# Kernel optimization log

Hardware: AMD Instinct MI355X
Metric: run time of the kernel (lower is better)

## Reference

```python
import jax, jax.numpy as jnp
import numpy as np

B, K, V, NB = 256, 62, 14522, 28

def setup_inputs() -> dict:
    key = jax.random.key(0)
    ks = jax.random.split(key, 10)
    thetas = jax.random.normal(ks[0], (B, K * 3), dtype=jnp.float32) * 0.2
    bone_lengths_core = jax.random.normal(ks[1], (B, NB), dtype=jnp.float32)
    center_bone_length = jax.random.uniform(ks[2], (B, 1), dtype=jnp.float32) + 0.5
    trans = jax.random.normal(ks[3], (B, 3), dtype=jnp.float32)
    scale = jax.random.uniform(ks[4], (B,), dtype=jnp.float32) + 0.5
    v_template = jax.random.normal(ks[5], (V, 3), dtype=jnp.float32) * 0.05
    t_pose_joints = jax.random.normal(ks[6], (K, 3), dtype=jnp.float32) * 0.1
    weights = jax.nn.softmax(jax.random.normal(ks[7], (V, K), dtype=jnp.float32) * 2.0, axis=1)
    # kinematic tree: parent[i] < i (binary-ish tree), parent[0] unused
    parents = jnp.maximum((jnp.arange(K) - 1) // 2, 0).astype(jnp.int64)
    bone_length_mapper = jax.random.randint(ks[8], (K,), -1, NB).astype(jnp.int64)
    return {"thetas": thetas, "bone_lengths_core": bone_lengths_core,
            "center_bone_length": center_bone_length, "trans": trans, "scale": scale,
            "v_template": v_template, "t_pose_joints": t_pose_joints, "weights": weights,
            "parents": parents, "bone_length_mapper": bone_length_mapper}

def euler2mat(r):
    # r: [N,3] ZYX euler angles -> [N,3,3]
    z, y, x = r[:, 0], r[:, 1], r[:, 2]
    cx, sx = jnp.cos(x), jnp.sin(x)
    cy, sy = jnp.cos(y), jnp.sin(y)
    cz, sz = jnp.cos(z), jnp.sin(z)
    one = jnp.ones_like(x)
    zero = jnp.zeros_like(x)
    Rx = jnp.stack([one, zero, zero, zero, cx, -sx, zero, sx, cx], -1).reshape(-1, 3, 3)
    Ry = jnp.stack([cy, zero, sy, zero, one, zero, -sy, zero, cy], -1).reshape(-1, 3, 3)
    Rz = jnp.stack([cz, -sz, zero, sz, cz, zero, zero, zero, one], -1).reshape(-1, 3, 3)
    return jnp.einsum('nij,njk,nkl->nil', Rz, Ry, Rx)

def _forward(thetas, bone_lengths_core, center_bone_length, trans, scale,
             v_template, t_pose_joints, weights, parents, bone_length_mapper):
    b = thetas.shape[0]
    k = t_pose_joints.shape[0]
    blc = jax.nn.sigmoid(bone_lengths_core / 5.0) * 2.0          # [B,28]
    R = euler2mat(thetas.reshape(-1, 3)).reshape(b, k, 3, 3)      # [B,K,3,3]
    Jt = t_pose_joints                                            # [K,3]
    # per-joint bone-length scale factor [B,K]
    gathered = blc[:, jnp.clip(bone_length_mapper, 0)]            # [B,K]
    factor = jnp.where(bone_length_mapper[None, :] < 0, 1.0, gathered)
    factor = factor.at[:, 1].set(center_bone_length[:, 0])
    factor = factor.at[:, 0].set(1.0)
    # local translations: root uses J0, others scaled offsets to parent
    off = (Jt - Jt[parents])[None] * factor[:, :, None]           # [B,K,3]
    off = off.at[:, 0].set(Jt[0][None])
    # local affines A [B,K,4,4]
    A = jnp.zeros((b, k, 4, 4), dtype=thetas.dtype)
    A = A.at[:, :, :3, :3].set(R)
    A = A.at[:, :, :3, 3].set(off)
    A = A.at[:, :, 3, 3].set(1.0)
    # compose along the kinematic tree
    G0 = jnp.zeros_like(A).at[:, 0].set(A[:, 0])
    def step(G_all, i):
        Gp = jnp.take(G_all, parents[i], axis=1)                  # [B,4,4]
        Gi = Gp @ jnp.take(A, i, axis=1)
        return jax.lax.dynamic_update_index_in_dim(G_all, Gi, i, axis=1), None
    G_all, _ = jax.lax.scan(step, G0, jnp.arange(1, k))
    J_final = G_all[:, :, :3, 3]                                  # [B,K,3]
    # subtract inverse-bind contribution: G' = G - pack(G @ [J;0])
    RJ = jnp.einsum('bkij,kj->bki', G_all[:, :, :3, :3], Jt)
    G = G_all.at[:, :, :3, 3].add(-RJ)
    # LBS skinning: T [B,V,4,4]
    T = jnp.einsum('bkij,vk->bvij', G, weights)
    rest_h = jnp.concatenate([v_template, jnp.ones((v_template.shape[0], 1), v_template.dtype)], axis=1)
    v = jnp.einsum('bvij,vj->bvi', T, rest_h)[:, :, :3]
    V_final = v * scale[:, None, None] + trans[:, None, :]
    J_out = J_final * scale[:, None, None] + trans[:, None, :]
    return V_final, J_out

def reference(thetas, bone_lengths_core, center_bone_length, trans, scale,
              v_template, t_pose_joints, weights, parents, bone_length_mapper):
    return _forward(thetas, bone_lengths_core, center_bone_length, trans, scale,
                    v_template, t_pose_joints, weights, parents, bone_length_mapper)
```

## Files before the change

kernel.cpp:

```cpp
#include <hip/hip_runtime.h>

#define NJ     62
#define NV     14522
#define NCORE  28
#define KPAD   256
#define OUTF   (NV * 3)
#define MT     908
#define NSTR   192

typedef __attribute__((ext_vector_type(8))) short short8v;
typedef __attribute__((ext_vector_type(4))) short short4v;
typedef __attribute__((ext_vector_type(4))) float floatx4;
typedef __attribute__((ext_vector_type(2))) float floatx2;

#define AS1(p) ((const __attribute__((address_space(1))) void*)(p))
#define AS3(p) ((__attribute__((address_space(3))) void*)(p))

#define SCHED0() __builtin_amdgcn_sched_barrier(0)
#define WAITVM0() do { SCHED0(); asm volatile("s_waitcnt vmcnt(0)" ::: "memory"); SCHED0(); } while (0)

static __device__ inline short f2bf(float x) {
    unsigned u = __float_as_uint(x);
    unsigned r = (u + 0x7fffu + ((u >> 16) & 1u)) >> 16;
    return (short)r;
}

static __device__ inline short8v pack8(float a0, float a1, float a2, float a3,
                                       float a4, float a5, float a6, float a7) {
    union { unsigned u[4]; short8v v; } p;
    asm("v_cvt_pk_bf16_f32 %0, %1, %2" : "=v"(p.u[0]) : "v"(a0), "v"(a1));
    asm("v_cvt_pk_bf16_f32 %0, %1, %2" : "=v"(p.u[1]) : "v"(a2), "v"(a3));
    asm("v_cvt_pk_bf16_f32 %0, %1, %2" : "=v"(p.u[2]) : "v"(a4), "v"(a5));
    asm("v_cvt_pk_bf16_f32 %0, %1, %2" : "=v"(p.u[3]) : "v"(a6), "v"(a7));
    return p.v;
}

static __device__ inline unsigned swz(unsigned off) {
    return off ^ (((off >> 9) & 7u) << 4);
}

__global__ __launch_bounds__(256) void fk_kernel(
    const float* __restrict__ thetas, const float* __restrict__ blc,
    const float* __restrict__ cbl, const float* __restrict__ trans,
    const float* __restrict__ scale, const float* __restrict__ tpose,
    const int* __restrict__ parents, const int* __restrict__ mapper,
    short* __restrict__ Bt, float* __restrict__ Jout)
{
    __shared__ float Asm[4][NJ][12];
    __shared__ float Gsm[4][NJ][12];

    const int w = threadIdx.x >> 6;
    const int b = blockIdx.x * 4 + w;
    const int k = threadIdx.x & 63;
    int p = 0;

    if (k < NJ) {
        p = parents[k];
        const float tz = thetas[(b * NJ + k) * 3 + 0];
        const float ty = thetas[(b * NJ + k) * 3 + 1];
        const float tx = thetas[(b * NJ + k) * 3 + 2];
        const float cx = cosf(tx), sx = sinf(tx);
        const float cy = cosf(ty), sy = sinf(ty);
        const float cz = cosf(tz), sz = sinf(tz);
        const float r00 = cz * cy;
        const float r01 = cz * sy * sx - sz * cx;
        const float r02 = sz * sx + cz * sy * cx;
        const float r10 = sz * cy;
        const float r11 = cz * cx + sz * sy * sx;
        const float r12 = sz * sy * cx - cz * sx;
        const float r20 = -sy;
        const float r21 = cy * sx;
        const float r22 = cy * cx;

        float f;
        const int m = mapper[k];
        if (k == 0)        f = 1.0f;
        else if (k == 1)   f = cbl[b];
        else if (m < 0)    f = 1.0f;
        else               f = 2.0f / (1.0f + expf(-blc[b * NCORE + m] * 0.2f));

        float ox, oy, oz;
        if (k == 0) {
            ox = tpose[0]; oy = tpose[1]; oz = tpose[2];
        } else {
            ox = (tpose[k * 3 + 0] - tpose[p * 3 + 0]) * f;
            oy = (tpose[k * 3 + 1] - tpose[p * 3 + 1]) * f;
            oz = (tpose[k * 3 + 2] - tpose[p * 3 + 2]) * f;
        }
        Asm[w][k][0] = r00; Asm[w][k][1] = r01; Asm[w][k][2]  = r02; Asm[w][k][3]  = ox;
        Asm[w][k][4] = r10; Asm[w][k][5] = r11; Asm[w][k][6]  = r12; Asm[w][k][7]  = oy;
        Asm[w][k][8] = r20; Asm[w][k][9] = r21; Asm[w][k][10] = r22; Asm[w][k][11] = oz;
    }
    __syncthreads();

    if (k == 0) {
        #pragma unroll
        for (int j = 0; j < 12; ++j) Gsm[w][0][j] = Asm[w][0][j];
    }
    __syncthreads();

    const int depth = (k < NJ) ? (31 - __clz((unsigned)(k + 1))) : 99;
    for (int d = 1; d <= 5; ++d) {
        if (depth == d) {
            float gp[12], a[12], g[12];
            #pragma unroll
            for (int j = 0; j < 12; ++j) { gp[j] = Gsm[w][p][j]; a[j] = Asm[w][k][j]; }
            #pragma unroll
            for (int i = 0; i < 3; ++i) {
                #pragma unroll
                for (int j = 0; j < 4; ++j) {
                    float s = (j == 3) ? gp[i * 4 + 3] : 0.0f;
                    s = fmaf(gp[i * 4 + 0], a[0 * 4 + j], s);
                    s = fmaf(gp[i * 4 + 1], a[1 * 4 + j], s);
                    s = fmaf(gp[i * 4 + 2], a[2 * 4 + j], s);
                    g[i * 4 + j] = s;
                }
            }
            #pragma unroll
            for (int j = 0; j < 12; ++j) Gsm[w][k][j] = g[j];
        }
        __syncthreads();
    }

    if (k < NJ) {
        float g[12];
        #pragma unroll
        for (int j = 0; j < 12; ++j) g[j] = Gsm[w][k][j];
        const float jx = tpose[k * 3 + 0];
        const float jy = tpose[k * 3 + 1];
        const float jz = tpose[k * 3 + 2];
        const float s  = scale[b];
        Jout[(b * NJ + k) * 3 + 0] = fmaf(g[3],  s, trans[b * 3 + 0]);
        Jout[(b * NJ + k) * 3 + 1] = fmaf(g[7],  s, trans[b * 3 + 1]);
        Jout[(b * NJ + k) * 3 + 2] = fmaf(g[11], s, trans[b * 3 + 2]);
        float np[3];
        np[0] = g[3]  - (g[0] * jx + g[1] * jy + g[2]  * jz);
        np[1] = g[7]  - (g[4] * jx + g[5] * jy + g[6]  * jz);
        np[2] = g[11] - (g[8] * jx + g[9] * jy + g[10] * jz);

        const int lkj = k >> 4;
        const int rr  = k & 15;
        const int qb  = 32 * (rr >> 1) + 8 * lkj + 4 * (rr & 1);
        #pragma unroll
        for (int i = 0; i < 3; ++i) {
            short4v o;
            o[0] = f2bf(g[i * 4 + 0]);
            o[1] = f2bf(g[i * 4 + 1]);
            o[2] = f2bf(g[i * 4 + 2]);
            o[3] = f2bf(np[i]);
            *(short4v*)&Bt[(size_t)(b * 3 + i) * KPAD + qb] = o;
        }
        if (k == 0) {
            short4v z = {0, 0, 0, 0};
            #pragma unroll
            for (int i = 0; i < 3; ++i) {
                *(short4v*)&Bt[(size_t)(b * 3 + i) * KPAD + 248] = z;
                *(short4v*)&Bt[(size_t)(b * 3 + i) * KPAD + 252] = z;
            }
        }
    }
}

__global__ __launch_bounds__(256, 3) void gemm_skin(
    const float* __restrict__ W,
    const float* __restrict__ vt,
    const short* __restrict__ Bt,
    const float* __restrict__ scale,
    const float* __restrict__ trans,
    float* __restrict__ out)
{
    __shared__ __align__(16) char ldsB[48 * 512];
    __shared__ __align__(16) float epi_all[4 * 1600];

    const int tid  = threadIdx.x;
    const int wave = tid >> 6;
    const int lane = tid & 63;
    const int lrow = lane & 15;
    const int lk   = lane >> 4;
    const int yy    = blockIdx.x / 48;
    const int inner = blockIdx.x - yy * 48;
    const int s     = inner * 4 + wave;
    const int start  = s * 4 + (s < 140 ? s : 140);
    const int ntiles = 4 + (s < 140 ? 1 : 0);
    const int b0 = yy * 16;
    float* epi0 = epi_all + wave * 1600;
    float* epi1 = epi0 + 800;

    {
        const char* Bsrc = (const char*)(Bt + (size_t)yy * 48 * KPAD);
        #pragma unroll
        for (int cc = 0; cc < 6; ++cc) {
            const unsigned Lb = (unsigned)(wave * 6144 + cc * 1024);
            __builtin_amdgcn_global_load_lds(AS1(Bsrc + swz(Lb + lane * 16)),
                                             AS3(ldsB + Lb), 16, 0, 0);
        }
    }

    float sv[3], tv[3]; int eoff[3];
    #pragma unroll
    for (int nt = 0; nt < 3; ++nt) {
        const int n_loc = nt * 16 + lrow;
        const int bl = n_loc / 3, ii = n_loc - bl * 3;
        eoff[nt] = bl * 50 + ii;
        sv[nt] = scale[b0 + bl];
        tv[nt] = trans[(b0 + bl) * 3 + ii];
    }
    unsigned bofs[3], bxor[3];
    #pragma unroll
    for (int nt = 0; nt < 3; ++nt) {
        const unsigned brow = nt * 16 + lrow;
        bofs[nt] = brow * 512;
        bxor[nt] = (brow & 7u) << 4;
    }

    auto do_store = [&](int tt, const float* ebuf) {
        const int m48 = (start + tt) * 48;
        const bool edge = (m48 + 48 > OUTF);
        #pragma unroll
        for (int it = 0; it < 6; ++it) {
            const int idx = it * 64 + lane;
            const int r = idx / 24, j = idx - r * 24;
            const floatx2 val = *(const floatx2*)&ebuf[r * 50 + 2 * j];
            const int pp = m48 + 2 * j;
            if (!edge || pp + 1 < OUTF)
                *(floatx2*)&out[(size_t)(b0 + r) * OUTF + pp] = val;
        }
    };

    floatx4 wc[4]; float hcx, hcy, hcz;
    {
        int vrow = start * 16 + lrow;
        if (vrow > NV - 1) vrow = NV - 1;
        const float* Wb = W + (size_t)vrow * NJ + lk * 16;
        wc[0] = *(const floatx4*)(Wb + 0);
        wc[1] = *(const floatx4*)(Wb + 4);
        wc[2] = *(const floatx4*)(Wb + 8);
        wc[3] = *(const floatx4*)(Wb + 12);
        hcx = vt[vrow * 3 + 0]; hcy = vt[vrow * 3 + 1]; hcz = vt[vrow * 3 + 2];
    }

    WAITVM0();
    __syncthreads();

    for (int t = 0; t < ntiles; ++t) {
        float* ecur = (t & 1) ? epi1 : epi0;

        if (t > 0) do_store(t - 1, (t & 1) ? epi0 : epi1);

        floatx4 wn[4]; float hnx = 0.f, hny = 0.f, hnz = 0.f;
        if (t + 1 < ntiles) {
            int vr = (start + t + 1) * 16 + lrow;
            if (vr > NV - 1) vr = NV - 1;
            const float* Wb = W + (size_t)vr * NJ + lk * 16;
            wn[0] = *(const floatx4*)(Wb + 0);
            wn[1] = *(const floatx4*)(Wb + 4);
            wn[2] = *(const floatx4*)(Wb + 8);
            wn[3] = *(const floatx4*)(Wb + 12);
            hnx = vt[vr * 3 + 0]; hny = vt[vr * 3 + 1]; hnz = vt[vr * 3 + 2];
        } else {
            wn[0] = wn[1] = wn[2] = wn[3] = (floatx4){0.f, 0.f, 0.f, 0.f};
        }

        floatx4 acc[3];
        #pragma unroll
        for (int nt = 0; nt < 3; ++nt) acc[nt] = (floatx4){0.f, 0.f, 0.f, 0.f};
        __builtin_amdgcn_s_setprio(1);
        #pragma unroll
        for (int k8 = 0; k8 < 8; ++k8) {
            float w0 = wc[k8 >> 1][2 * (k8 & 1)];
            float w1 = wc[k8 >> 1][2 * (k8 & 1) + 1];
            if (lk == 3 && k8 == 7) { w0 = 0.f; w1 = 0.f; }
            const short8v a = pack8(w0 * hcx, w0 * hcy, w0 * hcz, w0,
                                    w1 * hcx, w1 * hcy, w1 * hcz, w1);
            const unsigned cb = (unsigned)(k8 * 4 + lk) * 16;
            #pragma unroll
            for (int nt = 0; nt < 3; ++nt) {
                const short8v bf = *(const short8v*)(ldsB + bofs[nt] + (cb ^ bxor[nt]));
                acc[nt] = __builtin_amdgcn_mfma_f32_16x16x32_bf16(
                    a, bf, acc[nt], 0, 0, 0);
            }
        }
        __builtin_amdgcn_s_setprio(0);

        #pragma unroll
        for (int nt = 0; nt < 3; ++nt) {
            #pragma unroll
            for (int r = 0; r < 4; ++r)
                ecur[eoff[nt] + (lk * 4 + r) * 3] =
                    fmaf(acc[nt][r], sv[nt], tv[nt]);
        }

        wc[0] = wn[0]; wc[1] = wn[1]; wc[2] = wn[2]; wc[3] = wn[3];
        hcx = hnx; hcy = hny; hcz = hnz;
    }

    do_store(ntiles - 1, ((ntiles - 1) & 1) ? epi1 : epi0);
}

extern "C" void kernel_launch(void* const* d_in, const int* in_sizes, int n_in,
                              void* d_out, int out_size, void* d_ws, size_t ws_size,
                              hipStream_t stream)
{
    const float* thetas  = (const float*)d_in[0];
    const float* blc     = (const float*)d_in[1];
    const float* cbl     = (const float*)d_in[2];
    const float* trans   = (const float*)d_in[3];
    const float* scale   = (const float*)d_in[4];
    const float* vtempl  = (const float*)d_in[5];
    const float* tpose   = (const float*)d_in[6];
    const float* weights = (const float*)d_in[7];
    const int*   parents = (const int*)d_in[8];
    const int*   mapper  = (const int*)d_in[9];

    float* out  = (float*)d_out;
    float* Jout = out + (size_t)256 * NV * 3;

    short* Bt = (short*)d_ws;

    fk_kernel<<<64, 256, 0, stream>>>(thetas, blc, cbl, trans, scale, tpose,
                                      parents, mapper, Bt, Jout);
    gemm_skin<<<768, 256, 0, stream>>>(weights, vtempl, Bt, scale, trans, out);
}
```

Before: 24.95 us.

## Precompute bf16 weighted-vertex A operand in prep kernel instead of per-tile in GEMM

Adds extra blocks to the forward-kinematics kernel that compute the bf16 A-matrix (weight times rest vertex, plus weight) once per vertex and write it to workspace. The skinning GEMM then loads the packed bf16 fragments directly instead of loading fp32 weights and vertices and converting them in the inner loop. This is meant to remove repeated VALU multiply and convert work across the 48 batch-tile blocks, at the cost of an extra global write and read pass and more registers for the prefetched fragments.

```diff
diff --git a/kernel.cpp b/kernel.cpp
--- a/kernel.cpp
+++ b/kernel.cpp
@@ -6,7 +6,7 @@
 #define KPAD   256
 #define OUTF   (NV * 3)
 #define MT     908
-#define NSTR   192
+#define WHBLK  227
 
 typedef __attribute__((ext_vector_type(8))) short short8v;
 typedef __attribute__((ext_vector_type(4))) short short4v;
@@ -25,29 +25,47 @@
     return (short)r;
 }
 
-static __device__ inline short8v pack8(float a0, float a1, float a2, float a3,
-                                       float a4, float a5, float a6, float a7) {
-    union { unsigned u[4]; short8v v; } p;
-    asm("v_cvt_pk_bf16_f32 %0, %1, %2" : "=v"(p.u[0]) : "v"(a0), "v"(a1));
-    asm("v_cvt_pk_bf16_f32 %0, %1, %2" : "=v"(p.u[1]) : "v"(a2), "v"(a3));
-    asm("v_cvt_pk_bf16_f32 %0, %1, %2" : "=v"(p.u[2]) : "v"(a4), "v"(a5));
-    asm("v_cvt_pk_bf16_f32 %0, %1, %2" : "=v"(p.u[3]) : "v"(a6), "v"(a7));
-    return p.v;
-}
-
 static __device__ inline unsigned swz(unsigned off) {
     return off ^ (((off >> 9) & 7u) << 4);
 }
 
-__global__ __launch_bounds__(256) void fk_kernel(
+__global__ __launch_bounds__(256) void prep_kernel(
     const float* __restrict__ thetas, const float* __restrict__ blc,
     const float* __restrict__ cbl, const float* __restrict__ trans,
     const float* __restrict__ scale, const float* __restrict__ tpose,
     const int* __restrict__ parents, const int* __restrict__ mapper,
-    short* __restrict__ Bt, float* __restrict__ Jout)
+    const float* __restrict__ W, const float* __restrict__ vt,
+    short* __restrict__ Bt, short* __restrict__ WH,
+    float* __restrict__ Jout)
 {
     __shared__ float Asm[4][NJ][12];
     __shared__ float Gsm[4][NJ][12];
+
+    if (blockIdx.x >= 64) {
+        const int id = (blockIdx.x - 64) * 256 + threadIdx.x;
+        const int v  = id >> 2;
+        const int lk = id & 3;
+        if (v >= NV) return;
+        float wj[16];
+        #pragma unroll
+        for (int e = 0; e < 16; ++e) {
+            const int j = lk * 16 + e;
+            wj[e] = (j < NJ) ? W[(size_t)v * NJ + j] : 0.f;
+        }
+        const float hx = vt[v * 3 + 0], hy = vt[v * 3 + 1], hz = vt[v * 3 + 2];
+        short* dst = WH + (size_t)v * KPAD + lk * 8;
+        #pragma unroll
+        for (int k8 = 0; k8 < 8; ++k8) {
+            const float w0 = wj[2 * k8], w1 = wj[2 * k8 + 1];
+            short8v o;
+            o[0] = f2bf(w0 * hx); o[1] = f2bf(w0 * hy);
+            o[2] = f2bf(w0 * hz); o[3] = f2bf(w0);
+            o[4] = f2bf(w1 * hx); o[5] = f2bf(w1 * hy);
+            o[6] = f2bf(w1 * hz); o[7] = f2bf(w1);
+            *(short8v*)(dst + k8 * 32) = o;
+        }
+        return;
+    }
 
     const int w = threadIdx.x >> 6;
     const int b = blockIdx.x * 4 + w;
@@ -162,8 +180,7 @@
 }
 
 __global__ __launch_bounds__(256, 3) void gemm_skin(
-    const float* __restrict__ W,
-    const float* __restrict__ vt,
+    const short* __restrict__ WH,
     const short* __restrict__ Bt,
     const float* __restrict__ scale,
     const float* __restrict__ trans,
@@ -227,16 +244,14 @@
         }
     };
 
-    floatx4 wc[4]; float hcx, hcy, hcz;
+    short8v ac[8];
     {
         int vrow = start * 16 + lrow;
         if (vrow > NV - 1) vrow = NV - 1;
-        const float* Wb = W + (size_t)vrow * NJ + lk * 16;
-        wc[0] = *(const floatx4*)(Wb + 0);
-        wc[1] = *(const floatx4*)(Wb + 4);
-        wc[2] = *(const floatx4*)(Wb + 8);
-        wc[3] = *(const floatx4*)(Wb + 12);
-        hcx = vt[vrow * 3 + 0]; hcy = vt[vrow * 3 + 1]; hcz = vt[vrow * 3 + 2];
+        const short* WHr = WH + (size_t)vrow * KPAD + lk * 8;
+        #pragma unroll
+        for (int k8 = 0; k8 < 8; ++k8)
+            ac[k8] = *(const short8v*)(WHr + k8 * 32);
     }
 
     WAITVM0();
@@ -247,18 +262,18 @@
 
         if (t > 0) do_store(t - 1, (t & 1) ? epi0 : epi1);
 
-        floatx4 wn[4]; float hnx = 0.f, hny = 0.f, hnz = 0.f;
+        short8v an[8];
         if (t + 1 < ntiles) {
             int vr = (start + t + 1) * 16 + lrow;
             if (vr > NV - 1) vr = NV - 1;
-            const float* Wb = W + (size_t)vr * NJ + lk * 16;
-            wn[0] = *(const floatx4*)(Wb + 0);
-            wn[1] = *(const floatx4*)(Wb + 4);
-            wn[2] = *(const floatx4*)(Wb + 8);
-            wn[3] = *(const floatx4*)(Wb + 12);
-            hnx = vt[vr * 3 + 0]; hny = vt[vr * 3 + 1]; hnz = vt[vr * 3 + 2];
+            const short* WHr = WH + (size_t)vr * KPAD + lk * 8;
+            #pragma unroll
+            for (int k8 = 0; k8 < 8; ++k8)
+                an[k8] = *(const short8v*)(WHr + k8 * 32);
         } else {
-            wn[0] = wn[1] = wn[2] = wn[3] = (floatx4){0.f, 0.f, 0.f, 0.f};
+            #pragma unroll
+            for (int k8 = 0; k8 < 8; ++k8)
+                an[k8] = (short8v){0, 0, 0, 0, 0, 0, 0, 0};
         }
 
         floatx4 acc[3];
@@ -267,17 +282,12 @@
         __builtin_amdgcn_s_setprio(1);
         #pragma unroll
         for (int k8 = 0; k8 < 8; ++k8) {
-            float w0 = wc[k8 >> 1][2 * (k8 & 1)];
-            float w1 = wc[k8 >> 1][2 * (k8 & 1) + 1];
-            if (lk == 3 && k8 == 7) { w0 = 0.f; w1 = 0.f; }
-            const short8v a = pack8(w0 * hcx, w0 * hcy, w0 * hcz, w0,
-                                    w1 * hcx, w1 * hcy, w1 * hcz, w1);
             const unsigned cb = (unsigned)(k8 * 4 + lk) * 16;
             #pragma unroll
             for (int nt = 0; nt < 3; ++nt) {
                 const short8v bf = *(const short8v*)(ldsB + bofs[nt] + (cb ^ bxor[nt]));
                 acc[nt] = __builtin_amdgcn_mfma_f32_16x16x32_bf16(
-                    a, bf, acc[nt], 0, 0, 0);
+                    ac[k8], bf, acc[nt], 0, 0, 0);
             }
         }
         __builtin_amdgcn_s_setprio(0);
@@ -290,8 +300,8 @@
                     fmaf(acc[nt][r], sv[nt], tv[nt]);
         }
 
-        wc[0] = wn[0]; wc[1] = wn[1]; wc[2] = wn[2]; wc[3] = wn[3];
-        hcx = hnx; hcy = hny; hcz = hnz;
+        #pragma unroll
+        for (int k8 = 0; k8 < 8; ++k8) ac[k8] = an[k8];
     }
 
     do_store(ntiles - 1, ((ntiles - 1) & 1) ? epi1 : epi0);
@@ -316,8 +326,10 @@
     float* Jout = out + (size_t)256 * NV * 3;
 
     short* Bt = (short*)d_ws;
-
-    fk_kernel<<<64, 256, 0, stream>>>(thetas, blc, cbl, trans, scale, tpose,
-                                      parents, mapper, Bt, Jout);
-    gemm_skin<<<768, 256, 0, stream>>>(weights, vtempl, Bt, scale, trans, out);
-}
+    short* WH = Bt + (size_t)768 * KPAD;
+
+    prep_kernel<<<64 + WHBLK, 256, 0, stream>>>(
+        thetas, blc, cbl, trans, scale, tpose, parents, mapper,
+        weights, vtempl, Bt, WH, Jout);
+    gemm_skin<<<768, 256, 0, stream>>>(WH, Bt, scale, trans, out);
+}
```

New measurement: 62.08 us. 2.49x slower.
